# Optimization experiments

Measured on AMD Instinct MI355X. Metric: run time of the kernel, lower is better.

## Reference

```python
import jax, jax.numpy as jnp
import numpy as np
import math

IMAGE_C = 1
IMAGE_W = 28
PIXELS_PER_ROW = IMAGE_W * IMAGE_C
NUM_HEADS = 8
TOP_K = 96
WINDOW_SIZE = 128
NEG_INF = -jnp.inf


def _causal_2d_mask(T):
    idx = jnp.arange(T)
    q_i = (idx // PIXELS_PER_ROW)[:, None]
    q_j = (idx % PIXELS_PER_ROW // IMAGE_C)[:, None]
    q_c = (idx % IMAGE_C)[:, None]
    k_i = (idx // PIXELS_PER_ROW)[None, :]
    k_j = (idx % PIXELS_PER_ROW // IMAGE_C)[None, :]
    k_c = (idx % IMAGE_C)[None, :]
    allowed = (k_i < q_i) | ((k_i == q_i) & (k_j < q_j)) | ((k_i == q_i) & (k_j == q_j) & (k_c <= q_c))
    return jnp.where(allowed, 0.0, NEG_INF)[None, None]  # [1,1,T,T]


def _window_mask(T, window_size):
    idx = jnp.arange(T)
    blocked = idx[None, :] < idx[:, None] - window_size + 1
    return jnp.where(blocked, NEG_INF, 0.0)[None, None]  # [1,1,T,T]


def setup_inputs() -> dict:
    key = jax.random.key(0)
    ks = jax.random.split(key, 10)
    B, T, E = 4, 2048, 512
    H = NUM_HEADS
    s = 0.02
    return {
        "x": jax.random.normal(ks[0], (B, T, E), jnp.float32),
        "Wq": jax.random.normal(ks[1], (E, E), jnp.float32) * s,
        "bq": jnp.zeros((E,), jnp.float32),
        "Wk": jax.random.normal(ks[2], (E, E), jnp.float32) * s,
        "bk": jnp.zeros((E,), jnp.float32),
        "Wv": jax.random.normal(ks[3], (E, E), jnp.float32) * s,
        "bv": jnp.zeros((E,), jnp.float32),
        "Wo": jax.random.normal(ks[4], (E, E), jnp.float32) * s,
        "bo": jnp.zeros((E,), jnp.float32),
        "log_sigma": jnp.full((H, 1, 1), math.log(2.5), jnp.float32),
    }


def reference(x, Wq, bq, Wk, bk, Wv, bv, Wo, bo, log_sigma):
    B, T, E = x.shape
    H = NUM_HEADS
    D = E // H

    def split_heads(y):  # [B,T,E] -> [B,H,T,D]
        return y.reshape(B, T, H, D).transpose(0, 2, 1, 3)

    q = split_heads(x @ Wq.T + bq)
    k = split_heads(x @ Wk.T + bk)
    v = split_heads(x @ Wv.T + bv)

    # Gaussian-kernel (squared-distance) scores: ||q-k||^2 / (-2 sigma^2)
    q_sq = jnp.sum(q * q, axis=-1, keepdims=True)            # [B,H,T,1]
    k_sq = jnp.sum(k * k, axis=-1, keepdims=True).transpose(0, 1, 3, 2)  # [B,H,1,T]
    product = jnp.einsum("bhqd,bhkd->bhqk", q, k)
    dist_sq = q_sq + k_sq - 2.0 * product
    sigma_sq = jnp.exp(2.0 * log_sigma)                       # [H,1,1]
    scores = dist_sq / (-2.0 * sigma_sq)

    scores = scores + _causal_2d_mask(T)
    if WINDOW_SIZE < T:
        scores = scores + _window_mask(T, WINDOW_SIZE)

    if TOP_K < T:
        K_val = min(TOP_K, T)
        # keep only the top-K scores per row (threshold at the K-th value);
        # equivalent to torch's gather/scatter for distinct finite scores
        top_vals = jax.lax.top_k(scores, K_val)[0]            # [B,H,T,K]
        kth = top_vals[..., -1:]
        scores = jnp.where(scores >= kth, scores, NEG_INF)

    probs = jax.nn.softmax(scores, axis=-1)                   # dropout = identity (eval)
    out = jnp.einsum("bhqk,bhkd->bhqd", probs, v)
    out = out.transpose(0, 2, 1, 3).reshape(B, T, E)
    return out @ Wo.T + bo
```

## Files before the change

kernel.cpp:

```cpp
#include <hip/hip_runtime.h>
#include <math.h>

#define T_SEQ   2048
#define EDIM    512
#define NHEADS  8
#define DHEAD   64
#define BATCH   4
#define WIN     128
#define TOPK    96

typedef _Float16 f16;
typedef f16 f16x2 __attribute__((ext_vector_type(2)));
typedef f16 f16x4 __attribute__((ext_vector_type(4)));
typedef f16 f16x8 __attribute__((ext_vector_type(8)));
typedef float f32x4 __attribute__((ext_vector_type(4)));

#define GLD_LDS(gp, lp) \
    __builtin_amdgcn_global_load_lds((const __attribute__((address_space(1))) void*)(gp), \
                                     (__attribute__((address_space(3))) void*)(lp), 16, 0, 0)

__global__ __launch_bounds__(256) void convert_all(
    const float* __restrict__ x,  const float* __restrict__ wq,
    const float* __restrict__ wk, const float* __restrict__ wv,
    const float* __restrict__ wo,
    f16* __restrict__ xh, f16* __restrict__ wqkvh, f16* __restrict__ woh)
{
    long i = ((long)blockIdx.x * 256 + threadIdx.x) * 4;
    const float* src; f16* dst; long off;
    if      (i < 4194304L) { src = x;  dst = xh;             off = i;            }
    else if (i < 4456448L) { src = wq; dst = wqkvh;          off = i - 4194304L; }
    else if (i < 4718592L) { src = wk; dst = wqkvh + 262144; off = i - 4456448L; }
    else if (i < 4980736L) { src = wv; dst = wqkvh + 524288; off = i - 4718592L; }
    else                   { src = wo; dst = woh;            off = i - 4980736L; }
    float4 v = *(const float4*)(src + off);
    f16x4 h; h.x = (f16)v.x; h.y = (f16)v.y; h.z = (f16)v.z; h.w = (f16)v.w;
    *(f16x4*)(dst + off) = h;
}

__global__ __launch_bounds__(256) void gemm_qkv(
    const f16* __restrict__ A, const f16* __restrict__ W,
    const float* __restrict__ b0, const float* __restrict__ b1,
    const float* __restrict__ b2,
    f16* __restrict__ cq, f16* __restrict__ ck, f16* __restrict__ cv)
{
    __shared__ f16 SH[16384];
    f16* Ash = SH;
    f16* Bsh = SH + 8192;

    const int tid  = threadIdx.x;
    const int w    = tid >> 6;
    const int lane = tid & 63;
    const int m0   = blockIdx.x * 128;
    const int n0   = blockIdx.y * 128;
    const int K    = 512;
    const int lr   = lane & 15;
    const int lk8  = (lane >> 4) * 8;

    f32x4 acc[4][4];
#pragma unroll
    for (int i = 0; i < 4; i++)
#pragma unroll
        for (int j = 0; j < 4; j++) acc[i][j] = (f32x4){0.f, 0.f, 0.f, 0.f};

    const int wmi = (w & 1) * 4;
    const int wni = (w >> 1) * 4;

    for (int k0 = 0; k0 < K; k0 += 64) {
#pragma unroll
        for (int cc = 0; cc < 4; cc++) {
            const int c  = w * 4 + cc;
            const int ms = c & 7, kp = c >> 3;
            const int kcol = k0 + kp * 32 + lk8;
            GLD_LDS(A + (size_t)(m0 + ms * 16 + lr) * K + kcol, Ash + c * 512);
            GLD_LDS(W + (size_t)(n0 + ms * 16 + lr) * K + kcol, Bsh + c * 512);
        }
        __syncthreads();

#pragma unroll
        for (int kp = 0; kp < 2; kp++) {
            f16x8 af[4], bf[4];
#pragma unroll
            for (int i = 0; i < 4; i++)
                af[i] = *(const f16x8*)(Ash + (kp * 8 + wmi + i) * 512 + lane * 8);
#pragma unroll
            for (int j = 0; j < 4; j++)
                bf[j] = *(const f16x8*)(Bsh + (kp * 8 + wni + j) * 512 + lane * 8);
#pragma unroll
            for (int i = 0; i < 4; i++)
#pragma unroll
                for (int j = 0; j < 4; j++)
                    acc[i][j] = __builtin_amdgcn_mfma_f32_16x16x32_f16(af[i], bf[j], acc[i][j], 0, 0, 0);
        }
        __syncthreads();
    }

    const int quad = lane >> 4;
    const int mat  = n0 >> 9;
    const float* bias = (mat == 0) ? b0 : ((mat == 1) ? b1 : b2);
    const int bb  = m0 >> 11;
    const int t0  = m0 & (T_SEQ - 1);
    const int hh0 = (n0 & 511) >> 6;

    if (mat < 2) {
#pragma unroll
        for (int i = 0; i < 4; i++) {
#pragma unroll
            for (int j = 0; j < 4; j++) {
                const int nl = (w >> 1) * 64 + j * 16 + lr;
                const float bvv = bias[(n0 & 511) + nl];
#pragma unroll
                for (int r = 0; r < 4; r++) {
                    const int ml = (w & 1) * 64 + i * 16 + quad * 4 + r;
                    SH[ml * 128 + (nl ^ (((ml >> 2) & 7) << 4))] = (f16)(acc[i][j][r] + bvv);
                }
            }
        }
        __syncthreads();
        f16* dst = (mat == 0) ? cq : ck;
#pragma unroll
        for (int s = 0; s < 8; s++) {
            const int c   = tid + 256 * s;
            const int row = c >> 4;
            const int nt  = (c & 15) * 8;
            const f16x8 vv = *(const f16x8*)&SH[row * 128 + (nt ^ (((row >> 2) & 7) << 4))];
            const int hh = hh0 + (nt >> 6);
            const int dd = nt & 63;
            *(f16x8*)(dst + ((size_t)((bb * NHEADS + hh) * T_SEQ) + t0 + row) * 64 + dd) = vv;
        }
    } else {
#pragma unroll
        for (int i = 0; i < 4; i++) {
#pragma unroll
            for (int j = 0; j < 4; j++) {
                const int nl = (w >> 1) * 64 + j * 16 + lr;
                const float bvv = bias[(n0 & 511) + nl];
                const int mlb = (w & 1) * 64 + i * 16 + quad * 4;
                f16x4 pk;
#pragma unroll
                for (int r = 0; r < 4; r++) pk[r] = (f16)(acc[i][j][r] + bvv);
                *(f16x4*)&SH[nl * 128 + ((mlb + 8 * (nl & 15)) & 127)] = pk;
            }
        }
        __syncthreads();
#pragma unroll
        for (int s = 0; s < 8; s++) {
            const int c    = tid + 256 * s;
            const int nrow = c >> 4;
            const int cht  = c & 15;
            const int chl  = (cht + (nrow & 15)) & 15;
            const f16x8 vv = *(const f16x8*)&SH[nrow * 128 + chl * 8];
            const int hh = hh0 + (nrow >> 6);
            const int dd = nrow & 63;
            *(f16x8*)(cv + ((size_t)((bb * NHEADS + hh) * 64 + dd)) * T_SEQ + t0 + cht * 8) = vv;
        }
    }
}

__global__ __launch_bounds__(256) void gemm_o(
    const f16* __restrict__ A, const f16* __restrict__ W,
    const float* __restrict__ bias, float* __restrict__ C)
{
    __shared__ f16 Ash[16 * 512];
    __shared__ f16 Bsh[8 * 512];

    const int tid  = threadIdx.x;
    const int w    = tid >> 6;
    const int lane = tid & 63;
    const int m0   = blockIdx.x * 128;
    const int n0   = blockIdx.y * 64;
    const int lr   = lane & 15;
    const int lk8  = (lane >> 4) * 8;

    f32x4 acc[4][2];
#pragma unroll
    for (int i = 0; i < 4; i++)
#pragma unroll
        for (int j = 0; j < 2; j++) acc[i][j] = (f32x4){0.f, 0.f, 0.f, 0.f};

    for (int k0 = 0; k0 < 512; k0 += 64) {
#pragma unroll
        for (int cc = 0; cc < 4; cc++) {
            const int c  = w * 4 + cc;
            const int ms = c & 7, kp = c >> 3;
            GLD_LDS(A + (size_t)(m0 + ms * 16 + lr) * 512 + k0 + kp * 32 + lk8, Ash + c * 512);
        }
#pragma unroll
        for (int cc = 0; cc < 2; cc++) {
            const int c  = w * 2 + cc;
            const int ns = c & 3, kp = c >> 2;
            GLD_LDS(W + (size_t)(n0 + ns * 16 + lr) * 512 + k0 + kp * 32 + lk8, Bsh + c * 512);
        }
        __syncthreads();

#pragma unroll
        for (int kp = 0; kp < 2; kp++) {
            f16x8 af[4], bf[2];
#pragma unroll
            for (int i = 0; i < 4; i++)
                af[i] = *(const f16x8*)(Ash + (kp * 8 + (w & 1) * 4 + i) * 512 + lane * 8);
#pragma unroll
            for (int j = 0; j < 2; j++)
                bf[j] = *(const f16x8*)(Bsh + (kp * 4 + (w >> 1) * 2 + j) * 512 + lane * 8);
#pragma unroll
            for (int i = 0; i < 4; i++)
#pragma unroll
                for (int j = 0; j < 2; j++)
                    acc[i][j] = __builtin_amdgcn_mfma_f32_16x16x32_f16(af[i], bf[j], acc[i][j], 0, 0, 0);
        }
        __syncthreads();
    }

    const int quad = lane >> 4;
#pragma unroll
    for (int i = 0; i < 4; i++) {
#pragma unroll
        for (int j = 0; j < 2; j++) {
            const int n  = n0 + (w >> 1) * 32 + j * 16 + lr;
            const float bv = bias[n];
#pragma unroll
            for (int r = 0; r < 4; r++) {
                const int m = m0 + (w & 1) * 64 + i * 16 + quad * 4 + r;
                C[(size_t)m * 512 + n] = acc[i][j][r] + bv;
            }
        }
    }
}

__global__ __launch_bounds__(512, 4) void attn_v4(
    const f16* __restrict__ qh, const f16* __restrict__ kh,
    const f16* __restrict__ vtg, const float* __restrict__ logsig,
    f16* __restrict__ abh)
{
    __shared__ __align__(16) char smem[79616];
    f16*   Qs   = (f16*)smem;
    f16*   Ks   = (f16*)(smem + 11264);
    f16*   P    = (f16*)smem;
    float* Sc   = (float*)(smem + 45056);
    f16*   Vt   = (f16*)(smem + 45056);
    float* ksqs = (float*)(smem + 78848);

    const int tid = threadIdx.x, w = tid >> 6, lane = tid & 63;
    const int lr = lane & 15, quad = lane >> 4;
    const int q0 = blockIdx.x * 64, bh = blockIdx.y;
    const int h = bh & 7, b = bh >> 3;
    const size_t tb = (size_t)bh * T_SEQ;
    const int ks0 = q0 - 128;

    {
        const int row = tid >> 3, ch = tid & 7;
        f16x8 v = *(const f16x8*)(qh + (tb + q0 + row) * 64 + ch * 8);
        *(f16x8*)(Qs + row * 88 + ch * 8) = v;
    }
#pragma unroll
    for (int s = 0; s < 3; s++) {
        const int i = tid + 512 * s;
        const int row = i >> 3, ch = i & 7;
        const int kg = ks0 + row;
        f16x8 v = {};
        if (kg >= 0) v = *(const f16x8*)(kh + (tb + kg) * 64 + ch * 8);
        *(f16x8*)(Ks + row * 88 + ch * 8) = v;
        float ps = 0.f;
#pragma unroll
        for (int j = 0; j < 8; j++) { const float fv = (float)v[j]; ps += fv * fv; }
        ps += __shfl_xor(ps, 1);
        ps += __shfl_xor(ps, 2);
        ps += __shfl_xor(ps, 4);
        if (ch == 0) ksqs[row] = ps;
    }
    __syncthreads();

    const int mt  = w & 3;
    const int kh2 = w >> 2;
    f32x4 accQ[6];
#pragma unroll
    for (int jt = 0; jt < 6; jt++) accQ[jt] = (f32x4){0.f, 0.f, 0.f, 0.f};

#pragma unroll
    for (int kp = 0; kp < 2; kp++) {
        const f16x8 af = *(const f16x8*)(Qs + (mt * 16 + lr) * 88 + kp * 32 + quad * 8);
#pragma unroll
        for (int jt = 0; jt < 6; jt++) {
            const f16x8 bf = *(const f16x8*)(Ks + (kh2 * 96 + jt * 16 + lr) * 88 + kp * 32 + quad * 8);
            accQ[jt] = __builtin_amdgcn_mfma_f32_16x16x32_f16(af, bf, accQ[jt], 0, 0, 0);
        }
    }
    const float inv_s2 = __expf(-2.0f * logsig[h]);
#pragma unroll
    for (int jt = 0; jt < 6; jt++) {
        const int c  = kh2 * 96 + jt * 16 + lr;
        const float kq = ksqs[c];
        const int kg = ks0 + c;
#pragma unroll
        for (int r = 0; r < 4; r++) {
            const int dq = mt * 16 + quad * 4 + r;
            const unsigned wc = (unsigned)(c - dq - 1);
            if (wc < 128u) {
                Sc[dq * 132 + wc] = (kg >= 0) ? (accQ[jt][r] - 0.5f * kq) * inv_s2
                                              : -INFINITY;
            }
        }
    }
    __syncthreads();

    const int wq8 = w * 8;
#pragma unroll 1
    for (int g = 0; g < 2; g++) {
        const int dq0 = wq8 + g * 4;
        float s0[4], s1[4], m[4];
        unsigned u0[4], u1[4], t[4];
#pragma unroll
        for (int qq = 0; qq < 4; qq++) {
            const int dq = dq0 + qq;
            s0[qq] = Sc[dq * 132 + lane];
            s1[qq] = Sc[dq * 132 + 64 + lane];
            const unsigned b0 = __float_as_uint(s0[qq]);
            const unsigned b1 = __float_as_uint(s1[qq]);
            u0[qq] = b0 ^ (unsigned)(((int)b0 >> 31) | 0x80000000);
            u1[qq] = b1 ^ (unsigned)(((int)b1 >> 31) | 0x80000000);
            m[qq] = __uint_as_float(__builtin_amdgcn_readlane(__float_as_uint(s1[qq]), 63));
            t[qq] = 0u;
        }
#pragma unroll
        for (int bit = 31; bit >= 0; bit--) {
#pragma unroll
            for (int qq = 0; qq < 4; qq++) {
                const unsigned c = t[qq] | (1u << bit);
                const int n = __popcll(__ballot(u0[qq] >= c)) +
                              __popcll(__ballot(u1[qq] >= c));
                if (n >= TOPK) t[qq] = c;
            }
        }
#pragma unroll
        for (int qq = 0; qq < 4; qq++) {
            const int dq = dq0 + qq;
            const float p0 = (u0[qq] >= t[qq]) ? __expf(s0[qq] - m[qq]) : 0.f;
            const float p1 = (u1[qq] >= t[qq]) ? __expf(s1[qq] - m[qq]) : 0.f;
            P[dq * 216 + dq + 1 + lane]  = (f16)p0;
            P[dq * 216 + dq + 65 + lane] = (f16)p1;
            P[dq * 216 + ((lane <= dq) ? lane : lane + 128)] = (f16)0.f;
        }
    }
    __syncthreads();

#pragma unroll
    for (int s = 0; s < 3; s++) {
        const int i = tid + 512 * s;
        const int d = i / 24, ch = i % 24;
        const int t0 = ks0 + ch * 8;
        f16x8 vv = {};
        if (t0 >= 0) vv = *(const f16x8*)(vtg + ((size_t)bh * 64 + d) * T_SEQ + t0);
        *(f16x8*)(Vt + d * 216 + ch * 8) = vv;
    }
    __syncthreads();

    const int nh = w >> 2;
    f32x4 accO[2];
#pragma unroll
    for (int nt = 0; nt < 2; nt++) accO[nt] = (f32x4){0.f, 0.f, 0.f, 0.f};
    f32x4 accS = (f32x4){0.f, 0.f, 0.f, 0.f};
    f16x8 onesf;
#pragma unroll
    for (int j = 0; j < 8; j++) onesf[j] = (f16)1.0f;

#pragma unroll
    for (int ks = 0; ks < 6; ks++) {
        const f16x8 pf = *(const f16x8*)(P + (mt * 16 + lr) * 216 + ks * 32 + quad * 8);
#pragma unroll
        for (int nt = 0; nt < 2; nt++) {
            const f16x8 vf = *(const f16x8*)(Vt + (nh * 32 + nt * 16 + lr) * 216 + ks * 32 + quad * 8);
            accO[nt] = __builtin_amdgcn_mfma_f32_16x16x32_f16(pf, vf, accO[nt], 0, 0, 0);
        }
        accS = __builtin_amdgcn_mfma_f32_16x16x32_f16(pf, onesf, accS, 0, 0, 0);
    }
    float inv[4];
#pragma unroll
    for (int r = 0; r < 4; r++) inv[r] = 1.0f / accS[r];

#pragma unroll
    for (int nt = 0; nt < 2; nt++) {
        const int d = nh * 32 + nt * 16 + lr;
#pragma unroll
        for (int r = 0; r < 4; r++) {
            const int q = q0 + mt * 16 + quad * 4 + r;
            abh[((size_t)(b * T_SEQ + q)) * 512 + h * 64 + d] = (f16)(accO[nt][r] * inv[r]);
        }
    }
}

extern "C" void kernel_launch(void* const* d_in, const int* in_sizes, int n_in,
                              void* d_out, int out_size, void* d_ws, size_t ws_size,
                              hipStream_t stream)
{
    const float* x      = (const float*)d_in[0];
    const float* Wq     = (const float*)d_in[1];
    const float* bq     = (const float*)d_in[2];
    const float* Wk     = (const float*)d_in[3];
    const float* bk     = (const float*)d_in[4];
    const float* Wv     = (const float*)d_in[5];
    const float* bv     = (const float*)d_in[6];
    const float* Wo     = (const float*)d_in[7];
    const float* bo     = (const float*)d_in[8];
    const float* logsig = (const float*)d_in[9];

    f16* xh    = (f16*)d_ws;
    f16* wqkvh = xh + 4194304;
    f16* woh   = wqkvh + 786432;
    f16* qh    = woh + 262144;
    f16* kh    = qh + 4194304;
    f16* vtg   = kh + 4194304;
    f16* abh   = xh;

    convert_all<<<5120, 256, 0, stream>>>(x, Wq, Wk, Wv, Wo, xh, wqkvh, woh);

    gemm_qkv<<<dim3(64, 12), 256, 0, stream>>>(xh, wqkvh, bq, bk, bv, qh, kh, vtg);

    attn_v4<<<dim3(T_SEQ / 64, BATCH * NHEADS), 512, 0, stream>>>(
        qh, kh, vtg, logsig, abh);

    gemm_o<<<dim3(64, 8), 256, 0, stream>>>(abh, woh, bo, (float*)d_out);
}
```

Before: 172.9 us.

## Swizzle GEMM block order into M-bands and prefetch V tile early in attention

Both GEMMs now launch a 1D grid and remap block IDs so consecutive blocks cover 8 M-tiles by all N-tiles within a band. This is meant to improve L2 reuse of the A and weight tiles. The attention kernel issues the global loads for the V tile into registers at kernel start, then stores them to LDS after the softmax phase, hiding the V load latency behind score computation. The cost is 24 extra VGPRs per thread held across the main phase, which could raise register pressure under the 512x4 launch bound.

Result: slower. 177.4 us (+2.6%).

```diff
diff --git a/kernel.cpp b/kernel.cpp
--- a/kernel.cpp
+++ b/kernel.cpp
@@ -47,11 +47,15 @@
     f16* Ash = SH;
     f16* Bsh = SH + 8192;
 
+    const int bid  = blockIdx.x;
+    const int band = bid / 96;
+    const int rem  = bid - band * 96;
+    const int m0   = (band * 8 + (rem & 7)) * 128;
+    const int n0   = (rem >> 3) * 128;
+
     const int tid  = threadIdx.x;
     const int w    = tid >> 6;
     const int lane = tid & 63;
-    const int m0   = blockIdx.x * 128;
-    const int n0   = blockIdx.y * 128;
     const int K    = 512;
     const int lr   = lane & 15;
     const int lk8  = (lane >> 4) * 8;
@@ -163,11 +167,15 @@
     __shared__ f16 Ash[16 * 512];
     __shared__ f16 Bsh[8 * 512];
 
+    const int bid  = blockIdx.x;
+    const int band = bid >> 6;
+    const int rem  = bid & 63;
+    const int m0   = (band * 8 + (rem & 7)) * 128;
+    const int n0   = (rem >> 3) * 64;
+
     const int tid  = threadIdx.x;
     const int w    = tid >> 6;
     const int lane = tid & 63;
-    const int m0   = blockIdx.x * 128;
-    const int n0   = blockIdx.y * 64;
     const int lr   = lane & 15;
     const int lk8  = (lane >> 4) * 8;
 
@@ -226,7 +234,7 @@
     }
 }
 
-__global__ __launch_bounds__(512, 4) void attn_v4(
+__global__ __launch_bounds__(512, 4) void attn_v6(
     const f16* __restrict__ qh, const f16* __restrict__ kh,
     const f16* __restrict__ vtg, const float* __restrict__ logsig,
     f16* __restrict__ abh)
@@ -246,6 +254,18 @@
     const size_t tb = (size_t)bh * T_SEQ;
     const int ks0 = q0 - 128;
 
+    f16x8 vpre[3];
+    int vd[3], vch[3];
+#pragma unroll
+    for (int s = 0; s < 3; s++) {
+        const int i = tid + 512 * s;
+        vd[s] = i / 24; vch[s] = i % 24;
+        const int t0 = ks0 + vch[s] * 8;
+        f16x8 vv = {};
+        if (t0 >= 0) vv = *(const f16x8*)(vtg + ((size_t)bh * 64 + vd[s]) * T_SEQ + t0);
+        vpre[s] = vv;
+    }
+
     {
         const int row = tid >> 3, ch = tid & 7;
         f16x8 v = *(const f16x8*)(qh + (tb + q0 + row) * 64 + ch * 8);
@@ -343,14 +363,8 @@
     __syncthreads();
 
 #pragma unroll
-    for (int s = 0; s < 3; s++) {
-        const int i = tid + 512 * s;
-        const int d = i / 24, ch = i % 24;
-        const int t0 = ks0 + ch * 8;
-        f16x8 vv = {};
-        if (t0 >= 0) vv = *(const f16x8*)(vtg + ((size_t)bh * 64 + d) * T_SEQ + t0);
-        *(f16x8*)(Vt + d * 216 + ch * 8) = vv;
-    }
+    for (int s = 0; s < 3; s++)
+        *(f16x8*)(Vt + vd[s] * 216 + vch[s] * 8) = vpre[s];
     __syncthreads();
 
     const int nh = w >> 2;
@@ -412,10 +426,10 @@
 
     convert_all<<<5120, 256, 0, stream>>>(x, Wq, Wk, Wv, Wo, xh, wqkvh, woh);
 
-    gemm_qkv<<<dim3(64, 12), 256, 0, stream>>>(xh, wqkvh, bq, bk, bv, qh, kh, vtg);
-
-    attn_v4<<<dim3(T_SEQ / 64, BATCH * NHEADS), 512, 0, stream>>>(
+    gemm_qkv<<<768, 256, 0, stream>>>(xh, wqkvh, bq, bk, bv, qh, kh, vtg);
+
+    attn_v6<<<dim3(T_SEQ / 64, BATCH * NHEADS), 512, 0, stream>>>(
         qh, kh, vtg, logsig, abh);
 
-    gemm_o<<<dim3(64, 8), 256, 0, stream>>>(abh, woh, bo, (float*)d_out);
+    gemm_o<<<512, 256, 0, stream>>>(abh, woh, bo, (float*)d_out);
 }
```
